# Performance work log

Hardware: AMD Instinct MI355X
Metric: run time of the kernel (lower is better)

The kernel has to match this reference:

```python
import jax, jax.numpy as jnp
import numpy as np

B = 262144   # batch
L = 50       # sequence feature length (hardcoded in source loop)
H = 1024     # fc_hidden_size
E = 256      # embedding_dim
DROP_P = 0.2


def setup_inputs() -> dict:
    key = jax.random.key(0)
    k1, k2, k3, k4 = jax.random.split(key, 4)
    seq = jax.random.normal(k1, (B, 1, L), dtype=jnp.float32)
    # emulate -1 padding after a random valid length so the early-break path is exercised
    lengths = jax.random.randint(k2, (B,), 10, L + 1)
    pad = jnp.arange(L)[None, None, :] >= lengths[:, None, None]
    seq = jnp.where(pad, jnp.float32(-1.0), seq)
    W1 = jax.random.normal(k3, (L, H), dtype=jnp.float32) * np.float32(1.0 / np.sqrt(L))
    b1 = jnp.zeros((H,), dtype=jnp.float32)
    W2 = jax.random.normal(k4, (H, E), dtype=jnp.float32) * np.float32(1.0 / np.sqrt(H))
    b2 = jnp.zeros((E,), dtype=jnp.float32)
    return {"seq": seq, "W1": W1, "b1": b1, "W2": W2, "b2": b2}


def reference(seq, W1, b1, W2, b2):
    x = seq[:, 0, :]                                   # [B, L]
    # first position equal to -1 per row (loop breaks there); L if none
    is_neg = x == jnp.float32(-1.0)
    first_neg = jnp.where(is_neg.any(axis=-1), jnp.argmax(is_neg, axis=-1), L)  # [B]
    valid = jnp.arange(L)[None, :] < first_neg[:, None]                          # [B, L]
    # per-element Bernoulli(0.2) dropout applied only before the break point
    drop = jax.random.uniform(jax.random.key(42), x.shape) < DROP_P
    x = jnp.where(drop & valid, jnp.float32(0.0), x)
    # Linear -> ReLU -> Linear, then squeeze(1) (already squeezed above)
    h = jax.nn.relu(x @ W1 + b1)                       # [B, H]
    return h @ W2 + b2                                 # [B, E]
```

## Files before the change

kernel.cpp:

```cpp
#include <hip/hip_runtime.h>


typedef __attribute__((ext_vector_type(8))) short short8;
typedef __attribute__((ext_vector_type(4))) float f32x4;

__device__ __forceinline__ unsigned short f2bf(float f) {
  unsigned u = __float_as_uint(f);
  u += 0x7fffu + ((u >> 16) & 1u);
  return (unsigned short)(u >> 16);
}

__device__ __forceinline__ unsigned rotl_(unsigned x, int d) {
  return (x << d) | (x >> (32 - d));
}

__device__ __forceinline__ bool drop_rand(unsigned j) {
  const unsigned k0 = 0u, k1 = 42u, k2 = 0x1BD11BDAu ^ 42u;
  unsigned v0 = 0u + k0;
  unsigned v1 = j + k1;
#define MIX(rot) { v0 += v1; v1 = rotl_(v1, rot); v1 ^= v0; }
  MIX(13) MIX(15) MIX(26) MIX(6)   v0 += k1; v1 += k2 + 1u;
  MIX(17) MIX(29) MIX(16) MIX(24)  v0 += k2; v1 += k0 + 2u;
  MIX(13) MIX(15) MIX(26) MIX(6)   v0 += k0; v1 += k1 + 3u;
  MIX(17) MIX(29) MIX(16) MIX(24)  v0 += k1; v1 += k2 + 4u;
  MIX(13) MIX(15) MIX(26) MIX(6)   v0 += k2; v1 += k0 + 5u;
#undef MIX
  unsigned bits = v0 ^ v1;
  float u = __uint_as_float((bits >> 9) | 0x3f800000u) - 1.0f;
  return u < 0.2f;
}

__device__ __forceinline__ void gload_lds16(const unsigned short* g, unsigned short* l) {
  __builtin_amdgcn_global_load_lds(
      (const __attribute__((address_space(1))) unsigned int*)g,
      (__attribute__((address_space(3))) unsigned int*)l, 16, 0, 0);
}

__device__ __forceinline__ unsigned cvt_pk_bf16(float a, float b) {
  unsigned r;
  asm("v_cvt_pk_bf16_f32 %0, %1, %2" : "=v"(r) : "v"(a), "v"(b));
  return r;
}

__global__ void pack_weights(const float* __restrict__ W1, const float* __restrict__ W2,
                             unsigned short* __restrict__ ws) {
  int t = blockIdx.x * 256 + threadIdx.x;
  if (t < 8192) {
    int nblk = t >> 7, kb = (t >> 6) & 1, lane = t & 63;
    int kbase = kb * 32 + ((lane >> 4) * 8);
    int col = nblk * 16 + (lane & 15);
    short8 vv;
#pragma unroll
    for (int j = 0; j < 8; ++j) {
      int k = kbase + j;
      vv[j] = (short)((k < 50) ? f2bf(W1[k * 1024 + col]) : (unsigned short)0);
    }
    *(short8*)&ws[t * 8] = vv;
  } else {
    int t2 = t - 8192;
    int c = t2 >> 11, kb = (t2 >> 10) & 1, nt = (t2 >> 6) & 15, lane = t2 & 63;
    int kbase = c * 64 + kb * 32 + ((lane >> 4) * 8);
    int e = nt * 16 + (lane & 15);
    short8 vv;
#pragma unroll
    for (int j = 0; j < 8; ++j) vv[j] = (short)f2bf(W2[(size_t)(kbase + j) * 256 + e]);
    *(short8*)&ws[65536 + t2 * 8] = vv;
  }
}

__global__ __launch_bounds__(512, 4) void mlp_fused(
    const float* __restrict__ seq, const float* __restrict__ b1,
    const float* __restrict__ b2, const unsigned short* __restrict__ ws,
    float* __restrict__ out) {
  __shared__ __align__(16) unsigned short lds_h[8192];
  __shared__ __align__(16) unsigned short lds_w2[2][16384];

  const int tid  = threadIdx.x;
  const int lane = tid & 63;
  const int wave = tid >> 6;
  const int q    = lane >> 4;
  const int l15  = lane & 15;
  const int m0   = blockIdx.x * 128;
  const unsigned short* pW1 = ws;
  const unsigned short* pW2 = ws + 65536;

#pragma unroll
  for (int it = 0; it < 4; ++it)
    gload_lds16(&pW2[(size_t)(it * 512 + tid) * 8],
                &lds_w2[0][it * 4096 + wave * 512]);

  short8 xb[2];
  {
    const int row = m0 + wave * 16 + l15;
    const float* xrow = seq + (size_t)row * 50;
    float xv[2][8];
    unsigned long long nm = 0ull;
#pragma unroll
    for (int kb = 0; kb < 2; ++kb) {
#pragma unroll
      for (int jp = 0; jp < 4; ++jp) {
        const int k = kb * 32 + q * 8 + jp * 2;
        float2 v;
        if (k < 50) v = *(const float2*)&xrow[k];
        else        v = make_float2(0.f, 0.f);
        xv[kb][jp * 2]     = v.x;
        xv[kb][jp * 2 + 1] = v.y;
        if (v.x == -1.0f) nm |= 1ull << k;
        if (v.y == -1.0f) nm |= 1ull << (k + 1);
      }
    }
    nm |= __shfl_xor(nm, 16);
    nm |= __shfl_xor(nm, 32);
    const int fn   = nm ? __builtin_ctzll(nm) : 64;
    const int kmax = fn < 50 ? fn : 50;
    const unsigned jbase = (unsigned)row * 50u;
#pragma unroll
    for (int kb = 0; kb < 2; ++kb) {
      short8 vv;
#pragma unroll
      for (int j = 0; j < 8; ++j) {
        const int k = kb * 32 + q * 8 + j;
        float v = xv[kb][j];
        if (k < kmax && drop_rand(jbase + (unsigned)k)) v = 0.0f;
        vv[j] = (short)f2bf(v);
      }
      xb[kb] = vv;
    }
  }

  f32x4 acc[4][4];
#pragma unroll
  for (int mt = 0; mt < 4; ++mt)
#pragma unroll
    for (int ni = 0; ni < 4; ++ni) acc[mt][ni] = f32x4{0.f, 0.f, 0.f, 0.f};

  const int rg  = wave >> 2;
  const int cgr = wave & 3;

  for (int c = 0; c < 16; ++c) {
    const int par = c & 1;

    f32x4 hacc[4];
#pragma unroll
    for (int hi = 0; hi < 4; ++hi) hacc[hi] = f32x4{0.f, 0.f, 0.f, 0.f};
#pragma unroll
    for (int kb = 0; kb < 2; ++kb) {
      short8 wa[4];
#pragma unroll
      for (int hi = 0; hi < 4; ++hi)
        wa[hi] = *(const short8*)&pW1[(size_t)(((c * 4 + hi) * 2 + kb) * 64 + lane) * 8];
#pragma unroll
      for (int hi = 0; hi < 4; ++hi)
        hacc[hi] = __builtin_amdgcn_mfma_f32_16x16x32_bf16(wa[hi], xb[kb], hacc[hi], 0, 0, 0);
    }

    if (c < 15) {
      __builtin_amdgcn_sched_barrier(0);
#pragma unroll
      for (int it = 0; it < 4; ++it)
        gload_lds16(&pW2[(size_t)(c + 1) * 16384 + (size_t)(it * 512 + tid) * 8],
                    &lds_w2[par ^ 1][it * 4096 + wave * 512]);
      __builtin_amdgcn_sched_barrier(0);
    }

#pragma unroll
    for (int hi = 0; hi < 4; ++hi) {
      const f32x4 bv = *(const f32x4*)&b1[c * 64 + hi * 16 + q * 4];
      const float v0 = fmaxf(hacc[hi][0] + bv[0], 0.f);
      const float v1 = fmaxf(hacc[hi][1] + bv[1], 0.f);
      const float v2 = fmaxf(hacc[hi][2] + bv[2], 0.f);
      const float v3 = fmaxf(hacc[hi][3] + bv[3], 0.f);
      const unsigned w0 = cvt_pk_bf16(v0, v1);
      const unsigned w1 = cvt_pk_bf16(v2, v3);
      const int kbx  = hi >> 1;
      const int qp   = ((hi & 1) << 1) | (q >> 1);
      const int elem = (wave * 2 + kbx) * 64 + qp * 16 + l15;
      uint2 val; val.x = w0; val.y = w1;
      *(uint2*)&lds_h[elem * 8 + (q & 1) * 4] = val;
    }

    __builtin_amdgcn_sched_barrier(0);
    asm volatile("s_waitcnt lgkmcnt(0)" ::: "memory");
    __builtin_amdgcn_sched_barrier(0);
    __builtin_amdgcn_s_barrier();
    __builtin_amdgcn_sched_barrier(0);

#pragma unroll
    for (int kb = 0; kb < 2; ++kb) {
      short8 ha[4], wb[4];
#pragma unroll
      for (int mt = 0; mt < 4; ++mt)
        ha[mt] = *(const short8*)&lds_h[(size_t)(((rg * 4 + mt) * 2 + kb) * 64 + lane) * 8];
#pragma unroll
      for (int ni = 0; ni < 4; ++ni)
        wb[ni] = *(const short8*)&lds_w2[par][(size_t)((kb * 16 + cgr * 4 + ni) * 64 + lane) * 8];
#pragma unroll
      for (int mt = 0; mt < 4; ++mt)
#pragma unroll
        for (int ni = 0; ni < 4; ++ni)
          acc[mt][ni] = __builtin_amdgcn_mfma_f32_16x16x32_bf16(ha[mt], wb[ni],
                                                                acc[mt][ni], 0, 0, 0);
    }

    if (c < 15) {
      __builtin_amdgcn_sched_barrier(0);
      __builtin_amdgcn_s_barrier();
      __builtin_amdgcn_sched_barrier(0);
    }
  }

#pragma unroll
  for (int ni = 0; ni < 4; ++ni) {
    const int e = cgr * 64 + ni * 16 + l15;
    const float b2v = b2[e];
#pragma unroll
    for (int mt = 0; mt < 4; ++mt) {
      const int rbase = m0 + rg * 64 + mt * 16 + q * 4;
#pragma unroll
      for (int r = 0; r < 4; ++r)
        out[(size_t)(rbase + r) * 256 + e] = acc[mt][ni][r] + b2v;
    }
  }
}

extern "C" void kernel_launch(void* const* d_in, const int* in_sizes, int n_in,
                              void* d_out, int out_size, void* d_ws, size_t ws_size,
                              hipStream_t stream) {
  const float* seq = (const float*)d_in[0];
  const float* W1  = (const float*)d_in[1];
  const float* b1  = (const float*)d_in[2];
  const float* W2  = (const float*)d_in[3];
  const float* b2  = (const float*)d_in[4];
  unsigned short* ws = (unsigned short*)d_ws;
  float* out = (float*)d_out;

  hipLaunchKernelGGL(pack_weights, dim3(160), dim3(256), 0, stream, W1, W2, ws);
  hipLaunchKernelGGL(mlp_fused, dim3(2048), dim3(512), 0, stream, seq, b1, b2, ws, out);
}
```

Measured before the change: 494.1 us.

## Software-pipeline first GEMM chunk ahead of second GEMM and prefetch W2 two chunks ahead

The loop is restructured so the first-layer MFMA for chunk i+1 is issued right after the second-layer MFMAs for chunk i. The ReLU/bf16 pack into LDS is deferred until after a barrier, so the two GEMM stages can overlap instead of running back to back. The W2 chunk is now staged two iterations ahead, with both LDS buffers filled before the loop starts. The b1 bias is folded into the accumulator initial value instead of being added after the MFMAs. The costs are more live registers (hnext alongside acc) and a second barrier per iteration, which could reduce occupancy or add sync overhead.

```diff
diff --git a/kernel.cpp b/kernel.cpp
--- a/kernel.cpp
+++ b/kernel.cpp
@@ -88,6 +88,10 @@
   for (int it = 0; it < 4; ++it)
     gload_lds16(&pW2[(size_t)(it * 512 + tid) * 8],
                 &lds_w2[0][it * 4096 + wave * 512]);
+#pragma unroll
+  for (int it = 0; it < 4; ++it)
+    gload_lds16(&pW2[16384 + (size_t)(it * 512 + tid) * 8],
+                &lds_w2[1][it * 4096 + wave * 512]);
 
   short8 xb[2];
   {
@@ -128,6 +132,47 @@
     }
   }
 
+  f32x4 hnext[4];
+#define GEMM1_STEP(C)                                                                \
+  {                                                                                  \
+    const int c_ = (C);                                                              \
+    _Pragma("unroll")                                                                \
+    for (int hi = 0; hi < 4; ++hi)                                                   \
+      hnext[hi] = *(const f32x4*)&b1[c_ * 64 + hi * 16 + q * 4];                     \
+    _Pragma("unroll")                                                                \
+    for (int kb = 0; kb < 2; ++kb) {                                                 \
+      short8 wa[4];                                                                  \
+      _Pragma("unroll")                                                              \
+      for (int hi = 0; hi < 4; ++hi)                                                 \
+        wa[hi] = *(const short8*)&pW1[(size_t)(((c_ * 4 + hi) * 2 + kb) * 64 + lane) * 8]; \
+      _Pragma("unroll")                                                              \
+      for (int hi = 0; hi < 4; ++hi)                                                 \
+        hnext[hi] = __builtin_amdgcn_mfma_f32_16x16x32_bf16(wa[hi], xb[kb],          \
+                                                            hnext[hi], 0, 0, 0);     \
+    }                                                                                \
+  }
+
+#define PACK_STEP()                                                                  \
+  {                                                                                  \
+    _Pragma("unroll")                                                                \
+    for (int hi = 0; hi < 4; ++hi) {                                                 \
+      const float v0 = fmaxf(hnext[hi][0], 0.f);                                     \
+      const float v1 = fmaxf(hnext[hi][1], 0.f);                                     \
+      const float v2 = fmaxf(hnext[hi][2], 0.f);                                     \
+      const float v3 = fmaxf(hnext[hi][3], 0.f);                                     \
+      const unsigned w0 = cvt_pk_bf16(v0, v1);                                       \
+      const unsigned w1 = cvt_pk_bf16(v2, v3);                                       \
+      const int kbx  = hi >> 1;                                                      \
+      const int qp   = ((hi & 1) << 1) | (q >> 1);                                   \
+      const int elem = (wave * 2 + kbx) * 64 + qp * 16 + l15;                        \
+      uint2 val; val.x = w0; val.y = w1;                                             \
+      *(uint2*)&lds_h[elem * 8 + (q & 1) * 4] = val;                                 \
+    }                                                                                \
+  }
+
+  GEMM1_STEP(0)
+  PACK_STEP()
+
   f32x4 acc[4][4];
 #pragma unroll
   for (int mt = 0; mt < 4; ++mt)
@@ -137,53 +182,13 @@
   const int rg  = wave >> 2;
   const int cgr = wave & 3;
 
-  for (int c = 0; c < 16; ++c) {
-    const int par = c & 1;
-
-    f32x4 hacc[4];
-#pragma unroll
-    for (int hi = 0; hi < 4; ++hi) hacc[hi] = f32x4{0.f, 0.f, 0.f, 0.f};
-#pragma unroll
-    for (int kb = 0; kb < 2; ++kb) {
-      short8 wa[4];
-#pragma unroll
-      for (int hi = 0; hi < 4; ++hi)
-        wa[hi] = *(const short8*)&pW1[(size_t)(((c * 4 + hi) * 2 + kb) * 64 + lane) * 8];
-#pragma unroll
-      for (int hi = 0; hi < 4; ++hi)
-        hacc[hi] = __builtin_amdgcn_mfma_f32_16x16x32_bf16(wa[hi], xb[kb], hacc[hi], 0, 0, 0);
-    }
-
-    if (c < 15) {
-      __builtin_amdgcn_sched_barrier(0);
-#pragma unroll
-      for (int it = 0; it < 4; ++it)
-        gload_lds16(&pW2[(size_t)(c + 1) * 16384 + (size_t)(it * 512 + tid) * 8],
-                    &lds_w2[par ^ 1][it * 4096 + wave * 512]);
-      __builtin_amdgcn_sched_barrier(0);
-    }
-
-#pragma unroll
-    for (int hi = 0; hi < 4; ++hi) {
-      const f32x4 bv = *(const f32x4*)&b1[c * 64 + hi * 16 + q * 4];
-      const float v0 = fmaxf(hacc[hi][0] + bv[0], 0.f);
-      const float v1 = fmaxf(hacc[hi][1] + bv[1], 0.f);
-      const float v2 = fmaxf(hacc[hi][2] + bv[2], 0.f);
-      const float v3 = fmaxf(hacc[hi][3] + bv[3], 0.f);
-      const unsigned w0 = cvt_pk_bf16(v0, v1);
-      const unsigned w1 = cvt_pk_bf16(v2, v3);
-      const int kbx  = hi >> 1;
-      const int qp   = ((hi & 1) << 1) | (q >> 1);
-      const int elem = (wave * 2 + kbx) * 64 + qp * 16 + l15;
-      uint2 val; val.x = w0; val.y = w1;
-      *(uint2*)&lds_h[elem * 8 + (q & 1) * 4] = val;
-    }
-
-    __builtin_amdgcn_sched_barrier(0);
-    asm volatile("s_waitcnt lgkmcnt(0)" ::: "memory");
-    __builtin_amdgcn_sched_barrier(0);
-    __builtin_amdgcn_s_barrier();
-    __builtin_amdgcn_sched_barrier(0);
+  asm volatile("s_waitcnt lgkmcnt(0)" ::: "memory");
+  __builtin_amdgcn_s_barrier();
+  __builtin_amdgcn_sched_barrier(0);
+
+  for (int i = 0; i < 16; ++i) {
+    const int par = i & 1;
+    const unsigned short* w2cur = &lds_w2[par][0];
 
 #pragma unroll
     for (int kb = 0; kb < 2; ++kb) {
@@ -193,7 +198,7 @@
         ha[mt] = *(const short8*)&lds_h[(size_t)(((rg * 4 + mt) * 2 + kb) * 64 + lane) * 8];
 #pragma unroll
       for (int ni = 0; ni < 4; ++ni)
-        wb[ni] = *(const short8*)&lds_w2[par][(size_t)((kb * 16 + cgr * 4 + ni) * 64 + lane) * 8];
+        wb[ni] = *(const short8*)&w2cur[(size_t)((kb * 16 + cgr * 4 + ni) * 64 + lane) * 8];
 #pragma unroll
       for (int mt = 0; mt < 4; ++mt)
 #pragma unroll
@@ -202,12 +207,29 @@
                                                                 acc[mt][ni], 0, 0, 0);
     }
 
-    if (c < 15) {
+    if (i < 15) {
+      GEMM1_STEP(i + 1)
+
       __builtin_amdgcn_sched_barrier(0);
       __builtin_amdgcn_s_barrier();
       __builtin_amdgcn_sched_barrier(0);
-    }
-  }
+
+      if (i < 14) {
+#pragma unroll
+        for (int it = 0; it < 4; ++it)
+          gload_lds16(&pW2[(size_t)(i + 2) * 16384 + (size_t)(it * 512 + tid) * 8],
+                      &lds_w2[par][it * 4096 + wave * 512]);
+      }
+
+      PACK_STEP()
+
+      asm volatile("s_waitcnt lgkmcnt(0)" ::: "memory");
+      __builtin_amdgcn_s_barrier();
+      __builtin_amdgcn_sched_barrier(0);
+    }
+  }
+#undef GEMM1_STEP
+#undef PACK_STEP
 
 #pragma unroll
   for (int ni = 0; ni < 4; ++ni) {
```

Result: no change. 491.5 us (-0.5%).
